# Optimization experiments

Measured on AMD Instinct MI355X. Metric: run time of the kernel, lower is better.

Reference implementation:

```python
import jax, jax.numpy as jnp
import numpy as np

N, V, D, F, E, H = 10000, 4, 3, 128, 320000, 128
EDGE_IN = 2 * F + 2 * V  # node_features[senders] + node_features[receivers] + lengths_x^2 + lengths_y^2
NORM_CONST = 1.0


def setup_inputs() -> dict:
    key = jax.random.key(0)
    ks = jax.random.split(key, 20)
    w = lambda k, shape: jax.random.normal(k, shape, jnp.float32) * 0.05
    z = lambda n: jnp.zeros((n,), jnp.float32)
    return dict(
        node_positions=jax.random.normal(ks[0], (N, V, D), jnp.float32),
        node_vectors=jax.random.normal(ks[1], (N, V, D), jnp.float32),
        node_features=jax.random.normal(ks[2], (N, F), jnp.float32),
        senders=jax.random.randint(ks[3], (E,), 0, N),
        receivers=jax.random.randint(ks[4], (E,), 0, N),
        We0=w(ks[5], (EDGE_IN, H)), be0=z(H), We1=w(ks[6], (H, H)), be1=z(H),
        Winf=w(ks[7], (H, 1)), binf=z(1),
        Wx0=w(ks[8], (H, H)), bx0=z(H), Wx1=w(ks[9], (H, H)), bx1=z(H), Wxf=w(ks[10], (H, V)),
        Wy0=w(ks[11], (H, H)), by0=z(H), Wy1=w(ks[12], (H, H)), by1=z(H), Wyf=w(ks[13], (H, V)),
        Wh0=w(ks[14], (H + F, H)), bh0=z(H), Wh1=w(ks[15], (H, H)), bh1=z(H), Wh2=w(ks[16], (H, F)), bh2=z(F),
    )


def reference(node_positions, node_vectors, node_features, senders, receivers,
              We0, be0, We1, be1, Winf, binf,
              Wx0, bx0, Wx1, bx1, Wxf,
              Wy0, by0, Wy1, by1, Wyf,
              Wh0, bh0, Wh1, bh1, Wh2, bh2):
    act = jax.nn.silu
    n_nodes = node_positions.shape[0]
    avg = int(np.sqrt(receivers.shape[0]))  # avg_num_neighbours as in source

    def radial(coord):  # coord: [N, V, D]
        d = coord[receivers] - coord[senders]              # [E, V, D]
        l = jnp.sqrt(jnp.sum(d * d, axis=-1) + 1e-8)       # [E, V] safe_norm
        d = d / (NORM_CONST + l[:, :, None])               # normalize=True
        return l, d

    lx, dx = radial(node_positions)
    ly, dy = radial(node_vectors)

    ef = jnp.concatenate([node_features[senders], node_features[receivers],
                          lx ** 2, ly ** 2], axis=-1)      # [E, 264]
    m = act(act(ef @ We0 + be0) @ We1 + be1)               # phi_e, activate_final=True

    # phi_x: torso MLP + no-bias head, tanh
    px = jnp.tanh(act(act(m @ Wx0 + bx0) @ Wx1 + bx1) @ Wxf)          # [E, V]
    shifts_x = jax.ops.segment_sum(dx * px[:, :, None], receivers, num_segments=n_nodes) / avg

    # phi_y: torso MLP + no-bias head, tanh
    py = jnp.tanh(act(act(m @ Wy0 + by0) @ Wy1 + by1) @ Wyf)          # [E, V]
    shifts_y = jax.ops.segment_sum(dy * py[:, :, None], receivers, num_segments=n_nodes) / avg

    # attention gate on messages
    m = m * jax.nn.sigmoid(m @ Winf + binf)
    m_i = jax.ops.segment_sum(m, receivers, num_segments=n_nodes) / avg

    # phi_h (activate_final=False) + residual_h
    hin = jnp.concatenate([m_i, node_features], axis=-1)
    features_out = act(act(hin @ Wh0 + bh0) @ Wh1 + bh1) @ Wh2 + bh2 + node_features

    skip = shifts_y
    vectors_out = skip + node_vectors            # residual_y
    positions_out = shifts_x + node_positions    # x_update='x', residual_x
    return positions_out, vectors_out, features_out, skip
```

## Files before the change

### kernel.cpp

```cpp
#include <hip/hip_runtime.h>
#include <math.h>

#define NN 10000
#define EE 320000
#define TE 32
#define INV_AVG (1.0f / 565.0f)

#define OUT_POS 0
#define OUT_VEC 120000
#define OUT_FEAT 240000
#define OUT_SKIP 1520000
#define OUT_TOTAL 1640000

#define WS_WE0 0
#define WS_WE1 36864
#define WS_WX0 53248
#define WS_WX1 69632
#define WS_WY0 86016
#define WS_WY1 102400
#define WS_WH0 118784
#define WS_WH1 151552
#define WS_WH2 167936
#define WS_WXF 184320
#define WS_WYF 186368
#define WS_OFF_NF 376832
#define WS_OFF_SORT 2936832
#define WS_OFF_CNT  4216832
#define WS_OFF_CUR  4256832

typedef __attribute__((ext_vector_type(8))) short bfrag;
typedef __attribute__((ext_vector_type(4))) float f4acc;

__device__ __forceinline__ float siluf(float x) {
    return x * __builtin_amdgcn_rcpf(1.0f + __expf(-x));
}
__device__ __forceinline__ float tanh_fast(float x) {
    return 1.0f - 2.0f * __builtin_amdgcn_rcpf(__expf(2.0f * x) + 1.0f);
}
__device__ __forceinline__ float sigmoid_fast(float x) {
    return __builtin_amdgcn_rcpf(1.0f + __expf(-x));
}
__device__ __forceinline__ unsigned int cvt_pk_bf16(float lo, float hi) {
    unsigned int r;
    asm("v_cvt_pk_bf16_f32 %0, %1, %2" : "=v"(r) : "v"(lo), "v"(hi));
    return r;
}
__device__ __forceinline__ unsigned short f2bf(float x) {
    union { float f; unsigned int u; } c; c.f = x;
    unsigned int r = c.u + 0x7FFFu + ((c.u >> 16) & 1u);
    return (unsigned short)(r >> 16);
}
__device__ __forceinline__ float bf2f(unsigned short h) {
    union { unsigned int u; float f; } c; c.u = ((unsigned int)h) << 16; return c.f;
}

__global__ __launch_bounds__(256) void init_kernel(const float* __restrict__ pos,
                                                   float* __restrict__ out,
                                                   int* __restrict__ cnt)
{
    int idx = blockIdx.x * 256 + threadIdx.x;
    if (idx < OUT_TOTAL) out[idx] = (idx < 120000) ? pos[idx] : 0.0f;
    if (idx < NN) cnt[idx] = 0;
}

__global__ __launch_bounds__(256) void prep_all(
    const float* __restrict__ nf, unsigned short* __restrict__ nfb,
    const int* __restrict__ rcv, int* __restrict__ cnt,
    const float* __restrict__ We0, const float* __restrict__ be0,
    const float* __restrict__ We1,
    const float* __restrict__ Wx0, const float* __restrict__ Wx1,
    const float* __restrict__ Wy0, const float* __restrict__ Wy1,
    const float* __restrict__ Wh0, const float* __restrict__ Wh1,
    const float* __restrict__ Wh2,
    const float* __restrict__ Wxf, const float* __restrict__ Wyf,
    unsigned short* __restrict__ wsW)
{
    int tid = blockIdx.x * 256 + threadIdx.x;
    int i = tid * 8;
    if (i < NN * 128) {
        float4 a = *(const float4*)(nf + i);
        float4 b = *(const float4*)(nf + i + 4);
        uint4 pk;
        pk.x = cvt_pk_bf16(a.x, a.y);
        pk.y = cvt_pk_bf16(a.z, a.w);
        pk.z = cvt_pk_bf16(b.x, b.y);
        pk.w = cvt_pk_bf16(b.z, b.w);
        *(uint4*)(nfb + i) = pk;
    }
    int e = tid * 2;
    if (e < EE) {
        atomicAdd(cnt + rcv[e], 1);
        atomicAdd(cnt + rcv[e + 1], 1);
    }
    if (tid >= 23552) return;
    if (tid >= 23040) {
        const float* Wf = (tid < 23296) ? Wxf : Wyf;
        unsigned short* dst = wsW + ((tid < 23296) ? WS_WXF : WS_WYF);
        int rel = tid - ((tid < 23296) ? 23040 : 23296);
        int kc = rel >> 6, lane = rel & 63;
        int lhi = lane >> 4, llo = lane & 15;
        unsigned short* o = dst + ((kc * 64 + lane) << 3);
#pragma unroll
        for (int j = 0; j < 8; ++j) {
            int k = kc * 32 + lhi * 8 + j;
            o[j] = (llo < 4) ? f2bf(Wf[k * 4 + llo]) : (unsigned short)0;
        }
        return;
    }
    const float* W; unsigned short* dst; int Kact = 128, rel; int isWe0 = 0;
    if (tid < 4608)        { W = We0; dst = wsW + WS_WE0; Kact = 264; rel = tid; isWe0 = 1; }
    else if (tid < 14848)  {
        int r = tid - 4608; int m = r >> 11; rel = r & 2047;
        switch (m) {
            case 0: W = We1; dst = wsW + WS_WE1; break;
            case 1: W = Wx0; dst = wsW + WS_WX0; break;
            case 2: W = Wx1; dst = wsW + WS_WX1; break;
            case 3: W = Wy0; dst = wsW + WS_WY0; break;
            default: W = Wy1; dst = wsW + WS_WY1; break;
        }
    }
    else if (tid < 18944)  { W = Wh0; dst = wsW + WS_WH0; Kact = 256; rel = tid - 14848; }
    else if (tid < 20992)  { W = Wh1; dst = wsW + WS_WH1; rel = tid - 18944; }
    else                   { W = Wh2; dst = wsW + WS_WH2; rel = tid - 20992; }
    int lane = rel & 63, oc = (rel >> 6) & 7, kc = rel >> 9;
    int k0 = kc * 32 + ((lane >> 4) << 3);
    int col = oc * 16 + (lane & 15);
    unsigned short* o = dst + (((kc * 8 + oc) * 64 + lane) << 3);
#pragma unroll
    for (int j = 0; j < 8; ++j) {
        int k = k0 + j;
        unsigned short v = 0;
        if (k < Kact) v = f2bf(W[k * 128 + col]);
        else if (isWe0 && k == 264) v = f2bf(be0[col]);
        o[j] = v;
    }
}

__global__ __launch_bounds__(256) void scan_kernel(const int* __restrict__ cnt,
                                                   int* __restrict__ cursor)
{
    __shared__ int partial[256];
    int t = threadIdx.x;
    int base = t * 40;
    int s = 0;
#pragma unroll 8
    for (int i = 0; i < 40; ++i) { int b = base + i; if (b < NN) s += cnt[b]; }
    partial[t] = s;
    __syncthreads();
    for (int off = 1; off < 256; off <<= 1) {
        int v = 0;
        if (t >= off) v = partial[t - off];
        __syncthreads();
        if (t >= off) partial[t] += v;
        __syncthreads();
    }
    int run = (t ? partial[t - 1] : 0);
    for (int i = 0; i < 40; ++i) {
        int b = base + i;
        if (b < NN) { cursor[b] = run; run += cnt[b]; }
    }
}

__global__ __launch_bounds__(256) void scatter_sort_kernel(const int* __restrict__ rcv,
                                                           int* __restrict__ cursor,
                                                           int* __restrict__ sortedIdx)
{
    int e = blockIdx.x * 256 + threadIdx.x;
    if (e < EE) {
        int slot = atomicAdd(cursor + rcv[e], 1);
        sortedIdx[slot] = e;
    }
}

template<int KC, int MT, int NT>
__device__ __forceinline__ void gemm_lds(const unsigned short* __restrict__ fragW,
                                         const unsigned short* Bld, const int bstride,
                                         const int tile0, const int lane,
                                         f4acc acc[MT][NT])
{
    const int lhi = lane >> 4, llo = lane & 15;
#pragma unroll
    for (int kc = 0; kc < KC; ++kc) {
        bfrag b[NT];
#pragma unroll
        for (int nt = 0; nt < NT; ++nt)
            b[nt] = *(const bfrag*)(Bld + (nt * 16 + llo) * bstride + kc * 32 + lhi * 8);
#pragma unroll
        for (int i = 0; i < MT; ++i) {
            bfrag a = *(const bfrag*)(fragW + (((kc * 8 + tile0 + i) * 64 + lane) << 3));
#pragma unroll
            for (int nt = 0; nt < NT; ++nt)
                acc[i][nt] = __builtin_amdgcn_mfma_f32_16x16x32_bf16(a, b[nt], acc[i][nt], 0, 0, 0);
        }
    }
}

__device__ __forceinline__ void epilogue_silu(f4acc acc[2][2], const float* __restrict__ bias,
                                              unsigned short* Dld, int lane, int w)
{
    const int lhi = lane >> 4, llo = lane & 15;
#pragma unroll
    for (int i = 0; i < 2; ++i) {
        int ch = (w * 2 + i) * 16 + lhi * 4;
        float4 bv = *(const float4*)(bias + ch);
#pragma unroll
        for (int nt = 0; nt < 2; ++nt) {
            uint2 pk;
            pk.x = cvt_pk_bf16(siluf(acc[i][nt][0] + bv.x), siluf(acc[i][nt][1] + bv.y));
            pk.y = cvt_pk_bf16(siluf(acc[i][nt][2] + bv.z), siluf(acc[i][nt][3] + bv.w));
            *(uint2*)(Dld + (nt * 16 + llo) * 136 + ch) = pk;
        }
    }
}

__device__ __forceinline__ void epilogue_silu_nobias(f4acc acc[2][2],
                                                     unsigned short* Dld, int lane, int w)
{
    const int lhi = lane >> 4, llo = lane & 15;
#pragma unroll
    for (int i = 0; i < 2; ++i) {
        int ch = (w * 2 + i) * 16 + lhi * 4;
#pragma unroll
        for (int nt = 0; nt < 2; ++nt) {
            uint2 pk;
            pk.x = cvt_pk_bf16(siluf(acc[i][nt][0]), siluf(acc[i][nt][1]));
            pk.y = cvt_pk_bf16(siluf(acc[i][nt][2]), siluf(acc[i][nt][3]));
            *(uint2*)(Dld + (nt * 16 + llo) * 136 + ch) = pk;
        }
    }
}

__global__ __launch_bounds__(256, 6) void edge_kernel(
    const float* __restrict__ pos, const float* __restrict__ vec,
    const unsigned short* __restrict__ nfb,
    const int* __restrict__ snd, const int* __restrict__ rcv,
    const int* __restrict__ sortedIdx,
    const unsigned short* __restrict__ wsW,
    const float* __restrict__ be1,
    const float* __restrict__ Winf, const float* __restrict__ binf,
    const float* __restrict__ bx0, const float* __restrict__ bx1,
    const float* __restrict__ by0, const float* __restrict__ by1,
    float* outPos, float* outSkip, float* outFeat)
{
    __shared__ unsigned short L2T[TE * 40];
    __shared__ unsigned short H0[TE * 136];
    __shared__ unsigned short Hm[TE * 136];
    __shared__ float dstore[TE * 24];
    __shared__ float pxy[TE * 8];
    __shared__ float gateacc[TE];
    __shared__ int sidx[TE], ridx[TE];

    const int t = threadIdx.x;
    const int lane = t & 63, w = t >> 6;
    const int lhi = lane >> 4, llo = lane & 15;
    const int e_base = blockIdx.x * TE;

    if (t < TE) {
        int eid = sortedIdx[e_base + t];
        int sn = snd[eid], rn = rcv[eid];
        sidx[t] = sn; ridx[t] = rn;
#pragma unroll
        for (int tensor = 0; tensor < 2; ++tensor) {
            const float* c = tensor ? vec : pos;
#pragma unroll
            for (int v = 0; v < 4; ++v) {
                float d0 = c[rn * 12 + v * 3 + 0] - c[sn * 12 + v * 3 + 0];
                float d1 = c[rn * 12 + v * 3 + 1] - c[sn * 12 + v * 3 + 1];
                float d2 = c[rn * 12 + v * 3 + 2] - c[sn * 12 + v * 3 + 2];
                float ss = fmaf(d0, d0, fmaf(d1, d1, d2 * d2)) + 1e-8f;
                float l = sqrtf(ss);
                float inv = __builtin_amdgcn_rcpf(1.0f + l);
                L2T[t * 40 + tensor * 4 + v] = f2bf(ss);
                dstore[t * 24 + tensor * 12 + v * 3 + 0] = d0 * inv;
                dstore[t * 24 + tensor * 12 + v * 3 + 1] = d1 * inv;
                dstore[t * 24 + tensor * 12 + v * 3 + 2] = d2 * inv;
            }
        }
#pragma unroll
        for (int j = 0; j < 6; ++j)
            *(uint2*)(L2T + t * 40 + 8 + j * 4) = make_uint2(0u, 0u);
        L2T[t * 40 + 8] = 0x3F80u;
    }
    if (t >= 64 && t < 96) gateacc[t - 64] = 0.0f;
    __syncthreads();

    {
        const int sn0 = sidx[llo], sn1 = sidx[16 + llo];
        const int rn0 = ridx[llo], rn1 = ridx[16 + llo];
        const unsigned short* s0 = nfb + sn0 * 128 + lhi * 8;
        const unsigned short* s1 = nfb + sn1 * 128 + lhi * 8;
        const unsigned short* r0 = nfb + rn0 * 128 + lhi * 8;
        const unsigned short* r1 = nfb + rn1 * 128 + lhi * 8;
        const int mt0 = w * 2;
        f4acc acc[2][2];
#pragma unroll
        for (int i = 0; i < 2; ++i) { acc[i][0] = (f4acc){0.f,0.f,0.f,0.f}; acc[i][1] = (f4acc){0.f,0.f,0.f,0.f}; }
#pragma unroll
        for (int kc = 0; kc < 8; ++kc) {
            bfrag b0 = *(const bfrag*)((kc < 4 ? s0 : r0) + (kc & 3) * 32);
            bfrag b1 = *(const bfrag*)((kc < 4 ? s1 : r1) + (kc & 3) * 32);
#pragma unroll
            for (int i = 0; i < 2; ++i) {
                bfrag a = *(const bfrag*)(wsW + WS_WE0 + (((kc * 8 + mt0 + i) * 64 + lane) << 3));
                acc[i][0] = __builtin_amdgcn_mfma_f32_16x16x32_bf16(a, b0, acc[i][0], 0, 0, 0);
                acc[i][1] = __builtin_amdgcn_mfma_f32_16x16x32_bf16(a, b1, acc[i][1], 0, 0, 0);
            }
        }
        {
            bfrag b0 = *(const bfrag*)(L2T + llo * 40 + lhi * 8);
            bfrag b1 = *(const bfrag*)(L2T + (16 + llo) * 40 + lhi * 8);
#pragma unroll
            for (int i = 0; i < 2; ++i) {
                bfrag a = *(const bfrag*)(wsW + WS_WE0 + (((8 * 8 + mt0 + i) * 64 + lane) << 3));
                acc[i][0] = __builtin_amdgcn_mfma_f32_16x16x32_bf16(a, b0, acc[i][0], 0, 0, 0);
                acc[i][1] = __builtin_amdgcn_mfma_f32_16x16x32_bf16(a, b1, acc[i][1], 0, 0, 0);
            }
        }
        epilogue_silu_nobias(acc, H0, lane, w);
    }
    __syncthreads();

    {
        f4acc acc[2][2];
#pragma unroll
        for (int i = 0; i < 2; ++i) { acc[i][0] = (f4acc){0.f,0.f,0.f,0.f}; acc[i][1] = (f4acc){0.f,0.f,0.f,0.f}; }
        gemm_lds<4, 2, 2>(wsW + WS_WE1, H0, 136, w * 2, lane, acc);
        float gp0 = 0.0f, gp1 = 0.0f;
#pragma unroll
        for (int i = 0; i < 2; ++i) {
            int ch = (w * 2 + i) * 16 + lhi * 4;
            float4 bv = *(const float4*)(be1 + ch);
            float4 wg = *(const float4*)(Winf + ch);
#pragma unroll
            for (int nt = 0; nt < 2; ++nt) {
                float v0 = siluf(acc[i][nt][0] + bv.x);
                float v1 = siluf(acc[i][nt][1] + bv.y);
                float v2 = siluf(acc[i][nt][2] + bv.z);
                float v3 = siluf(acc[i][nt][3] + bv.w);
                uint2 pk;
                pk.x = cvt_pk_bf16(v0, v1);
                pk.y = cvt_pk_bf16(v2, v3);
                *(uint2*)(Hm + (nt * 16 + llo) * 136 + ch) = pk;
                float g = fmaf(v0, wg.x, fmaf(v1, wg.y, fmaf(v2, wg.z, v3 * wg.w)));
                if (nt == 0) gp0 += g; else gp1 += g;
            }
        }
        gp0 += __shfl_xor(gp0, 16); gp0 += __shfl_xor(gp0, 32);
        gp1 += __shfl_xor(gp1, 16); gp1 += __shfl_xor(gp1, 32);
        if (lane < 16) {
            atomicAdd(&gateacc[lane], gp0);
            atomicAdd(&gateacc[16 + lane], gp1);
        }
    }
    __syncthreads();

#pragma unroll 1
    for (int br = 0; br < 2; ++br) {
        {
            const unsigned short* fw = wsW + (br ? WS_WY0 : WS_WX0);
            const float* bias = br ? by0 : bx0;
            f4acc acc[2][2];
#pragma unroll
            for (int i = 0; i < 2; ++i) { acc[i][0] = (f4acc){0.f,0.f,0.f,0.f}; acc[i][1] = (f4acc){0.f,0.f,0.f,0.f}; }
            gemm_lds<4, 2, 2>(fw, Hm, 136, w * 2, lane, acc);
            epilogue_silu(acc, bias, H0, lane, w);
        }
        __syncthreads();
        {
            const unsigned short* fw = wsW + (br ? WS_WY1 : WS_WX1);
            const float* bias = br ? by1 : bx1;
            f4acc acc[2][2];
#pragma unroll
            for (int i = 0; i < 2; ++i) { acc[i][0] = (f4acc){0.f,0.f,0.f,0.f}; acc[i][1] = (f4acc){0.f,0.f,0.f,0.f}; }
            gemm_lds<4, 2, 2>(fw, H0, 136, w * 2, lane, acc);
            __syncthreads();
            epilogue_silu(acc, bias, H0, lane, w);
        }
        __syncthreads();
        if (w < 2) {
            const unsigned short* fw = wsW + (br ? WS_WYF : WS_WXF);
            f4acc h = (f4acc){0.f, 0.f, 0.f, 0.f};
#pragma unroll
            for (int kc = 0; kc < 4; ++kc) {
                bfrag b = *(const bfrag*)(H0 + (w * 16 + llo) * 136 + kc * 32 + lhi * 8);
                bfrag a = *(const bfrag*)(fw + ((kc * 64 + lane) << 3));
                h = __builtin_amdgcn_mfma_f32_16x16x32_bf16(a, b, h, 0, 0, 0);
            }
            if (lhi == 0) {
#pragma unroll
                for (int v = 0; v < 4; ++v)
                    pxy[(w * 16 + llo) * 8 + br * 4 + v] = h[v];
            }
        }
        __syncthreads();
    }

    pxy[t] = tanh_fast(pxy[t]) * INV_AVG;
    if (t < TE) gateacc[t] = sigmoid_fast(gateacc[t] + binf[0]) * INV_AVG;
    __syncthreads();

    if (t < 128) {
        int half = t >> 6, pair = t & 63;
        int jj = pair * 2;
        int e0h = half * 16;
        float a0 = 0.0f, a1 = 0.0f;
        int prev_r = ridx[e0h];
#pragma unroll
        for (int i = 0; i < 16; ++i) {
            int e = e0h + i;
            int r = ridx[e];
            if (r != prev_r) {
                atomicAdd(outFeat + prev_r * 128 + jj, a0);
                atomicAdd(outFeat + prev_r * 128 + jj + 1, a1);
                a0 = a1 = 0.0f;
                prev_r = r;
            }
            unsigned int pk = *(const unsigned int*)(Hm + e * 136 + jj);
            float g = gateacc[e];
            a0 = fmaf(bf2f((unsigned short)(pk & 0xffffu)), g, a0);
            a1 = fmaf(bf2f((unsigned short)(pk >> 16)), g, a1);
        }
        atomicAdd(outFeat + prev_r * 128 + jj, a0);
        atomicAdd(outFeat + prev_r * 128 + jj + 1, a1);
    } else if (t >= 208) {
        int s = t - 208;
        int c = s >> 1, half = s & 1;
        int tensor = (c >= 12) ? 1 : 0;
        int rem = c - tensor * 12;
        int v = rem / 3;
        float* dstp = tensor ? outSkip : outPos;
        int e0h = half * 16;
        float acc = 0.0f;
        int prev_r = ridx[e0h];
#pragma unroll
        for (int i = 0; i < 16; ++i) {
            int e = e0h + i;
            int r = ridx[e];
            if (r != prev_r) {
                atomicAdd(dstp + prev_r * 12 + rem, acc);
                acc = 0.0f;
                prev_r = r;
            }
            acc = fmaf(dstore[e * 24 + c], pxy[e * 8 + tensor * 4 + v], acc);
        }
        atomicAdd(dstp + prev_r * 12 + rem, acc);
    }
}

__global__ __launch_bounds__(256) void node_kernel(
    const float* __restrict__ nf, const unsigned short* __restrict__ nfb,
    const float* __restrict__ nvec,
    const unsigned short* __restrict__ wsW,
    const float* __restrict__ bh0, const float* __restrict__ bh1,
    const float* __restrict__ bh2,
    float* outFeat , float* outVec,
    const float* __restrict__ outSkip)
{
    __shared__ unsigned short A[TE * 264];
    __shared__ unsigned short H1[TE * 136];
    __shared__ unsigned short H2[TE * 136];
    const int t = threadIdx.x;
    const int lane = t & 63, w = t >> 6;
    const int lhi = lane >> 4, llo = lane & 15;
    const int n_base = blockIdx.x * TE;

#pragma unroll
    for (int it = 0; it < 8; ++it) {
        int idx = t + it * 256;
        int row = idx >> 6, q = idx & 63;
        int n = n_base + row;
        float2 v = make_float2(0.f, 0.f);
        if (n < NN) v = *(const float2*)(outFeat + n * 128 + q * 2);
        *(unsigned int*)(A + row * 264 + q * 2) = cvt_pk_bf16(v.x, v.y);
    }
#pragma unroll
    for (int it = 0; it < 2; ++it) {
        int idx = t + it * 256;
        int row = idx >> 4, q = idx & 15;
        int n = n_base + row;
        uint4 v = make_uint4(0u, 0u, 0u, 0u);
        if (n < NN) v = *(const uint4*)(nfb + n * 128 + q * 8);
        *(uint4*)(A + row * 264 + 128 + q * 8) = v;
    }
    __syncthreads();
    {
        f4acc acc[2][2];
#pragma unroll
        for (int i = 0; i < 2; ++i) { acc[i][0] = (f4acc){0.f,0.f,0.f,0.f}; acc[i][1] = (f4acc){0.f,0.f,0.f,0.f}; }
        gemm_lds<8, 2, 2>(wsW + WS_WH0, A, 264, w * 2, lane, acc);
        epilogue_silu(acc, bh0, H1, lane, w);
    }
    __syncthreads();
    {
        f4acc acc[2][2];
#pragma unroll
        for (int i = 0; i < 2; ++i) { acc[i][0] = (f4acc){0.f,0.f,0.f,0.f}; acc[i][1] = (f4acc){0.f,0.f,0.f,0.f}; }
        gemm_lds<4, 2, 2>(wsW + WS_WH1, H1, 136, w * 2, lane, acc);
        epilogue_silu(acc, bh1, H2, lane, w);
    }
    __syncthreads();
    {
        f4acc acc[2][2];
#pragma unroll
        for (int i = 0; i < 2; ++i) { acc[i][0] = (f4acc){0.f,0.f,0.f,0.f}; acc[i][1] = (f4acc){0.f,0.f,0.f,0.f}; }
        gemm_lds<4, 2, 2>(wsW + WS_WH2, H2, 136, w * 2, lane, acc);
#pragma unroll
        for (int i = 0; i < 2; ++i) {
            int ch = (w * 2 + i) * 16 + lhi * 4;
            float4 bv = *(const float4*)(bh2 + ch);
#pragma unroll
            for (int nt = 0; nt < 2; ++nt) {
                int n = n_base + nt * 16 + llo;
                if (n < NN) {
                    float4 r = *(const float4*)(nf + n * 128 + ch);
                    float4 o;
                    o.x = acc[i][nt][0] + bv.x + r.x;
                    o.y = acc[i][nt][1] + bv.y + r.y;
                    o.z = acc[i][nt][2] + bv.z + r.z;
                    o.w = acc[i][nt][3] + bv.w + r.w;
                    *(float4*)(outFeat + n * 128 + ch) = o;
                }
            }
        }
    }
    {
        int idx = t;
        if (idx < TE * 12) {
            int n = n_base + idx / 12;
            if (n < NN) {
                int g = n_base * 12 + idx;
                outVec[g] = outSkip[g] + nvec[g];
            }
        }
        idx = t + 256;
        if (idx < TE * 12) {
            int n = n_base + idx / 12;
            if (n < NN) {
                int g = n_base * 12 + idx;
                outVec[g] = outSkip[g] + nvec[g];
            }
        }
    }
}

extern "C" void kernel_launch(void* const* d_in, const int* in_sizes, int n_in,
                              void* d_out, int out_size, void* d_ws, size_t ws_size,
                              hipStream_t stream)
{
    (void)in_sizes; (void)n_in; (void)out_size; (void)ws_size;

    const float* pos  = (const float*)d_in[0];
    const float* vecv = (const float*)d_in[1];
    const float* nf   = (const float*)d_in[2];
    const int*   snd  = (const int*)d_in[3];
    const int*   rcv  = (const int*)d_in[4];
    const float* We0  = (const float*)d_in[5];
    const float* be0  = (const float*)d_in[6];
    const float* We1  = (const float*)d_in[7];
    const float* be1  = (const float*)d_in[8];
    const float* Winf = (const float*)d_in[9];
    const float* binf = (const float*)d_in[10];
    const float* Wx0  = (const float*)d_in[11];
    const float* bx0  = (const float*)d_in[12];
    const float* Wx1  = (const float*)d_in[13];
    const float* bx1  = (const float*)d_in[14];
    const float* Wxf  = (const float*)d_in[15];
    const float* Wy0  = (const float*)d_in[16];
    const float* by0  = (const float*)d_in[17];
    const float* Wy1  = (const float*)d_in[18];
    const float* by1  = (const float*)d_in[19];
    const float* Wyf  = (const float*)d_in[20];
    const float* Wh0  = (const float*)d_in[21];
    const float* bh0  = (const float*)d_in[22];
    const float* Wh1  = (const float*)d_in[23];
    const float* bh1  = (const float*)d_in[24];
    const float* Wh2  = (const float*)d_in[25];
    const float* bh2  = (const float*)d_in[26];

    float* out     = (float*)d_out;
    float* outPos  = out + OUT_POS;
    float* outVec  = out + OUT_VEC;
    float* outFeat = out + OUT_FEAT;
    float* outSkip = out + OUT_SKIP;

    char* ws = (char*)d_ws;
    unsigned short* wsW = (unsigned short*)ws;
    unsigned short* nfb = (unsigned short*)(ws + WS_OFF_NF);
    int* sortedIdx      = (int*)(ws + WS_OFF_SORT);
    int* cnt            = (int*)(ws + WS_OFF_CNT);
    int* cursor         = (int*)(ws + WS_OFF_CUR);

    init_kernel<<<(OUT_TOTAL + 255) / 256, 256, 0, stream>>>(pos, out, cnt);

    prep_all<<<(NN * 128 / 8 + 255) / 256, 256, 0, stream>>>(
        nf, nfb, rcv, cnt,
        We0, be0, We1, Wx0, Wx1, Wy0, Wy1, Wh0, Wh1, Wh2, Wxf, Wyf, wsW);

    scan_kernel<<<1, 256, 0, stream>>>(cnt, cursor);
    scatter_sort_kernel<<<(EE + 255) / 256, 256, 0, stream>>>(rcv, cursor, sortedIdx);

    edge_kernel<<<EE / TE, 256, 0, stream>>>(
        pos, vecv, nfb, snd, rcv, sortedIdx, wsW,
        be1, Winf, binf,
        bx0, bx1, by0, by1,
        outPos, outSkip, outFeat);

    node_kernel<<<(NN + TE - 1) / TE, 256, 0, stream>>>(
        nf, nfb, vecv, wsW, bh0, bh1, bh2,
        outFeat, outVec, outSkip);
}
```

Before: 251.2 us.

## Use wave-shuffle scan, unroll edge MLP branches with extra LDS buffer, halve node tile

The single-block scan now runs 1024 threads and uses wave shuffles instead of a barrier-heavy LDS Hillis-Steele loop. In the edge kernel the x/y branch loop is unrolled, and a third LDS buffer removes the mid-GEMM barrier and lets the x head projection overlap with the y first layer. The occupancy hint drops from 6 to 4 blocks per CU. The node kernel tile shrinks from 32 to 16 nodes for more blocks, at the cost of less weight reuse per block.

Measured after the change: 258.7 us. 1.03x slower.

```diff
diff --git a/kernel.cpp b/kernel.cpp
--- a/kernel.cpp
+++ b/kernel.cpp
@@ -4,6 +4,7 @@
 #define NN 10000
 #define EE 320000
 #define TE 32
+#define TN 16
 #define INV_AVG (1.0f / 565.0f)
 
 #define OUT_POS 0
@@ -136,28 +137,45 @@
     }
 }
 
-__global__ __launch_bounds__(256) void scan_kernel(const int* __restrict__ cnt,
-                                                   int* __restrict__ cursor)
-{
-    __shared__ int partial[256];
+__global__ __launch_bounds__(1024) void scan_kernel(const int* __restrict__ cnt,
+                                                    int* __restrict__ cursor)
+{
+    __shared__ int wsum[16];
     int t = threadIdx.x;
-    int base = t * 40;
+    int lane = t & 63, wid = t >> 6;
+    int base = t * 10;
+    int c[10];
     int s = 0;
-#pragma unroll 8
-    for (int i = 0; i < 40; ++i) { int b = base + i; if (b < NN) s += cnt[b]; }
-    partial[t] = s;
-    __syncthreads();
-    for (int off = 1; off < 256; off <<= 1) {
-        int v = 0;
-        if (t >= off) v = partial[t - off];
-        __syncthreads();
-        if (t >= off) partial[t] += v;
-        __syncthreads();
-    }
-    int run = (t ? partial[t - 1] : 0);
-    for (int i = 0; i < 40; ++i) {
+#pragma unroll
+    for (int i = 0; i < 10; ++i) {
         int b = base + i;
-        if (b < NN) { cursor[b] = run; run += cnt[b]; }
+        c[i] = (b < NN) ? cnt[b] : 0;
+        s += c[i];
+    }
+    int run = s;
+#pragma unroll
+    for (int off = 1; off < 64; off <<= 1) {
+        int v = __shfl_up(run, off);
+        if (lane >= off) run += v;
+    }
+    if (lane == 63) wsum[wid] = run;
+    __syncthreads();
+    if (t < 16) {
+        int v = wsum[t];
+#pragma unroll
+        for (int off = 1; off < 16; off <<= 1) {
+            int u = __shfl_up(v, off);
+            if (t >= off) v += u;
+        }
+        wsum[t] = v;
+    }
+    __syncthreads();
+    int wave_excl = (wid == 0) ? 0 : wsum[wid - 1];
+    int excl = wave_excl + run - s;
+#pragma unroll
+    for (int i = 0; i < 10; ++i) {
+        int b = base + i;
+        if (b < NN) { cursor[b] = excl; excl += c[i]; }
     }
 }
 
@@ -195,8 +213,9 @@
     }
 }
 
-__device__ __forceinline__ void epilogue_silu(f4acc acc[2][2], const float* __restrict__ bias,
-                                              unsigned short* Dld, int lane, int w)
+template<int NT>
+__device__ __forceinline__ void epilogue_silu_t(f4acc acc[2][NT], const float* __restrict__ bias,
+                                                unsigned short* Dld, int lane, int w)
 {
     const int lhi = lane >> 4, llo = lane & 15;
 #pragma unroll
@@ -204,7 +223,7 @@
         int ch = (w * 2 + i) * 16 + lhi * 4;
         float4 bv = *(const float4*)(bias + ch);
 #pragma unroll
-        for (int nt = 0; nt < 2; ++nt) {
+        for (int nt = 0; nt < NT; ++nt) {
             uint2 pk;
             pk.x = cvt_pk_bf16(siluf(acc[i][nt][0] + bv.x), siluf(acc[i][nt][1] + bv.y));
             pk.y = cvt_pk_bf16(siluf(acc[i][nt][2] + bv.z), siluf(acc[i][nt][3] + bv.w));
@@ -230,7 +249,7 @@
     }
 }
 
-__global__ __launch_bounds__(256, 6) void edge_kernel(
+__global__ __launch_bounds__(256, 4) void edge_kernel(
     const float* __restrict__ pos, const float* __restrict__ vec,
     const unsigned short* __restrict__ nfb,
     const int* __restrict__ snd, const int* __restrict__ rcv,
@@ -245,6 +264,7 @@
     __shared__ unsigned short L2T[TE * 40];
     __shared__ unsigned short H0[TE * 136];
     __shared__ unsigned short Hm[TE * 136];
+    __shared__ unsigned short H2[TE * 136];
     __shared__ float dstore[TE * 24];
     __shared__ float pxy[TE * 8];
     __shared__ float gateacc[TE];
@@ -354,46 +374,71 @@
     }
     __syncthreads();
 
-#pragma unroll 1
-    for (int br = 0; br < 2; ++br) {
-        {
-            const unsigned short* fw = wsW + (br ? WS_WY0 : WS_WX0);
-            const float* bias = br ? by0 : bx0;
-            f4acc acc[2][2];
-#pragma unroll
-            for (int i = 0; i < 2; ++i) { acc[i][0] = (f4acc){0.f,0.f,0.f,0.f}; acc[i][1] = (f4acc){0.f,0.f,0.f,0.f}; }
-            gemm_lds<4, 2, 2>(fw, Hm, 136, w * 2, lane, acc);
-            epilogue_silu(acc, bias, H0, lane, w);
-        }
-        __syncthreads();
-        {
-            const unsigned short* fw = wsW + (br ? WS_WY1 : WS_WX1);
-            const float* bias = br ? by1 : bx1;
-            f4acc acc[2][2];
-#pragma unroll
-            for (int i = 0; i < 2; ++i) { acc[i][0] = (f4acc){0.f,0.f,0.f,0.f}; acc[i][1] = (f4acc){0.f,0.f,0.f,0.f}; }
-            gemm_lds<4, 2, 2>(fw, H0, 136, w * 2, lane, acc);
-            __syncthreads();
-            epilogue_silu(acc, bias, H0, lane, w);
-        }
-        __syncthreads();
+    {
+        f4acc acc[2][2];
+#pragma unroll
+        for (int i = 0; i < 2; ++i) { acc[i][0] = (f4acc){0.f,0.f,0.f,0.f}; acc[i][1] = (f4acc){0.f,0.f,0.f,0.f}; }
+        gemm_lds<4, 2, 2>(wsW + WS_WX0, Hm, 136, w * 2, lane, acc);
+        epilogue_silu_t<2>(acc, bx0, H0, lane, w);
+    }
+    __syncthreads();
+
+    {
+        f4acc acc[2][2];
+#pragma unroll
+        for (int i = 0; i < 2; ++i) { acc[i][0] = (f4acc){0.f,0.f,0.f,0.f}; acc[i][1] = (f4acc){0.f,0.f,0.f,0.f}; }
+        gemm_lds<4, 2, 2>(wsW + WS_WX1, H0, 136, w * 2, lane, acc);
+        epilogue_silu_t<2>(acc, bx1, H2, lane, w);
+    }
+    __syncthreads();
+
+    {
+        f4acc acc[2][2];
+#pragma unroll
+        for (int i = 0; i < 2; ++i) { acc[i][0] = (f4acc){0.f,0.f,0.f,0.f}; acc[i][1] = (f4acc){0.f,0.f,0.f,0.f}; }
+        gemm_lds<4, 2, 2>(wsW + WS_WY0, Hm, 136, w * 2, lane, acc);
+        epilogue_silu_t<2>(acc, by0, H0, lane, w);
         if (w < 2) {
-            const unsigned short* fw = wsW + (br ? WS_WYF : WS_WXF);
             f4acc h = (f4acc){0.f, 0.f, 0.f, 0.f};
 #pragma unroll
             for (int kc = 0; kc < 4; ++kc) {
-                bfrag b = *(const bfrag*)(H0 + (w * 16 + llo) * 136 + kc * 32 + lhi * 8);
-                bfrag a = *(const bfrag*)(fw + ((kc * 64 + lane) << 3));
+                bfrag b = *(const bfrag*)(H2 + (w * 16 + llo) * 136 + kc * 32 + lhi * 8);
+                bfrag a = *(const bfrag*)(wsW + WS_WXF + ((kc * 64 + lane) << 3));
                 h = __builtin_amdgcn_mfma_f32_16x16x32_bf16(a, b, h, 0, 0, 0);
             }
             if (lhi == 0) {
 #pragma unroll
                 for (int v = 0; v < 4; ++v)
-                    pxy[(w * 16 + llo) * 8 + br * 4 + v] = h[v];
-            }
-        }
-        __syncthreads();
-    }
+                    pxy[(w * 16 + llo) * 8 + v] = h[v];
+            }
+        }
+    }
+    __syncthreads();
+
+    {
+        f4acc acc[2][2];
+#pragma unroll
+        for (int i = 0; i < 2; ++i) { acc[i][0] = (f4acc){0.f,0.f,0.f,0.f}; acc[i][1] = (f4acc){0.f,0.f,0.f,0.f}; }
+        gemm_lds<4, 2, 2>(wsW + WS_WY1, H0, 136, w * 2, lane, acc);
+        epilogue_silu_t<2>(acc, by1, H2, lane, w);
+    }
+    __syncthreads();
+
+    if (w < 2) {
+        f4acc h = (f4acc){0.f, 0.f, 0.f, 0.f};
+#pragma unroll
+        for (int kc = 0; kc < 4; ++kc) {
+            bfrag b = *(const bfrag*)(H2 + (w * 16 + llo) * 136 + kc * 32 + lhi * 8);
+            bfrag a = *(const bfrag*)(wsW + WS_WYF + ((kc * 64 + lane) << 3));
+            h = __builtin_amdgcn_mfma_f32_16x16x32_bf16(a, b, h, 0, 0, 0);
+        }
+        if (lhi == 0) {
+#pragma unroll
+            for (int v = 0; v < 4; ++v)
+                pxy[(w * 16 + llo) * 8 + 4 + v] = h[v];
+        }
+    }
+    __syncthreads();
 
     pxy[t] = tanh_fast(pxy[t]) * INV_AVG;
     if (t < TE) gateacc[t] = sigmoid_fast(gateacc[t] + binf[0]) * INV_AVG;
@@ -456,16 +501,16 @@
     float* outFeat , float* outVec,
     const float* __restrict__ outSkip)
 {
-    __shared__ unsigned short A[TE * 264];
-    __shared__ unsigned short H1[TE * 136];
-    __shared__ unsigned short H2[TE * 136];
+    __shared__ unsigned short A[TN * 264];
+    __shared__ unsigned short H1[TN * 136];
+    __shared__ unsigned short H2b[TN * 136];
     const int t = threadIdx.x;
     const int lane = t & 63, w = t >> 6;
     const int lhi = lane >> 4, llo = lane & 15;
-    const int n_base = blockIdx.x * TE;
-
-#pragma unroll
-    for (int it = 0; it < 8; ++it) {
+    const int n_base = blockIdx.x * TN;
+
+#pragma unroll
+    for (int it = 0; it < 4; ++it) {
         int idx = t + it * 256;
         int row = idx >> 6, q = idx & 63;
         int n = n_base + row;
@@ -473,10 +518,8 @@
         if (n < NN) v = *(const float2*)(outFeat + n * 128 + q * 2);
         *(unsigned int*)(A + row * 264 + q * 2) = cvt_pk_bf16(v.x, v.y);
     }
-#pragma unroll
-    for (int it = 0; it < 2; ++it) {
-        int idx = t + it * 256;
-        int row = idx >> 4, q = idx & 15;
+    {
+        int row = t >> 4, q = t & 15;
         int n = n_base + row;
         uint4 v = make_uint4(0u, 0u, 0u, 0u);
         if (n < NN) v = *(const uint4*)(nfb + n * 128 + q * 8);
@@ -484,61 +527,44 @@
     }
     __syncthreads();
     {
-        f4acc acc[2][2];
-#pragma unroll
-        for (int i = 0; i < 2; ++i) { acc[i][0] = (f4acc){0.f,0.f,0.f,0.f}; acc[i][1] = (f4acc){0.f,0.f,0.f,0.f}; }
-        gemm_lds<8, 2, 2>(wsW + WS_WH0, A, 264, w * 2, lane, acc);
-        epilogue_silu(acc, bh0, H1, lane, w);
-    }
-    __syncthreads();
-    {
-        f4acc acc[2][2];
-#pragma unroll
-        for (int i = 0; i < 2; ++i) { acc[i][0] = (f4acc){0.f,0.f,0.f,0.f}; acc[i][1] = (f4acc){0.f,0.f,0.f,0.f}; }
-        gemm_lds<4, 2, 2>(wsW + WS_WH1, H1, 136, w * 2, lane, acc);
-        epilogue_silu(acc, bh1, H2, lane, w);
-    }
-    __syncthreads();
-    {
-        f4acc acc[2][2];
-#pragma unroll
-        for (int i = 0; i < 2; ++i) { acc[i][0] = (f4acc){0.f,0.f,0.f,0.f}; acc[i][1] = (f4acc){0.f,0.f,0.f,0.f}; }
-        gemm_lds<4, 2, 2>(wsW + WS_WH2, H2, 136, w * 2, lane, acc);
+        f4acc acc[2][1];
+        acc[0][0] = (f4acc){0.f,0.f,0.f,0.f}; acc[1][0] = (f4acc){0.f,0.f,0.f,0.f};
+        gemm_lds<8, 2, 1>(wsW + WS_WH0, A, 264, w * 2, lane, acc);
+        epilogue_silu_t<1>(acc, bh0, H1, lane, w);
+    }
+    __syncthreads();
+    {
+        f4acc acc[2][1];
+        acc[0][0] = (f4acc){0.f,0.f,0.f,0.f}; acc[1][0] = (f4acc){0.f,0.f,0.f,0.f};
+        gemm_lds<4, 2, 1>(wsW + WS_WH1, H1, 136, w * 2, lane, acc);
+        epilogue_silu_t<1>(acc, bh1, H2b, lane, w);
+    }
+    __syncthreads();
+    {
+        f4acc acc[2][1];
+        acc[0][0] = (f4acc){0.f,0.f,0.f,0.f}; acc[1][0] = (f4acc){0.f,0.f,0.f,0.f};
+        gemm_lds<4, 2, 1>(wsW + WS_WH2, H2b, 136, w * 2, lane, acc);
 #pragma unroll
         for (int i = 0; i < 2; ++i) {
             int ch = (w * 2 + i) * 16 + lhi * 4;
             float4 bv = *(const float4*)(bh2 + ch);
-#pragma unroll
-            for (int nt = 0; nt < 2; ++nt) {
-                int n = n_base + nt * 16 + llo;
-                if (n < NN) {
-                    float4 r = *(const float4*)(nf + n * 128 + ch);
-                    float4 o;
-                    o.x = acc[i][nt][0] + bv.x + r.x;
-                    o.y = acc[i][nt][1] + bv.y + r.y;
-                    o.z = acc[i][nt][2] + bv.z + r.z;
-                    o.w = acc[i][nt][3] + bv.w + r.w;
-                    *(float4*)(outFeat + n * 128 + ch) = o;
-                }
-            }
-        }
-    }
-    {
-        int idx = t;
-        if (idx < TE * 12) {
-            int n = n_base + idx / 12;
+            int n = n_base + llo;
             if (n < NN) {
-                int g = n_base * 12 + idx;
-                outVec[g] = outSkip[g] + nvec[g];
-            }
-        }
-        idx = t + 256;
-        if (idx < TE * 12) {
-            int n = n_base + idx / 12;
-            if (n < NN) {
-                int g = n_base * 12 + idx;
-                outVec[g] = outSkip[g] + nvec[g];
-            }
+                float4 r = *(const float4*)(nf + n * 128 + ch);
+                float4 o;
+                o.x = acc[i][0][0] + bv.x + r.x;
+                o.y = acc[i][0][1] + bv.y + r.y;
+                o.z = acc[i][0][2] + bv.z + r.z;
+                o.w = acc[i][0][3] + bv.w + r.w;
+                *(float4*)(outFeat + n * 128 + ch) = o;
+            }
+        }
+    }
+    if (t < TN * 12) {
+        int n = n_base + t / 12;
+        if (n < NN) {
+            int g = n_base * 12 + t;
+            outVec[g] = outSkip[g] + nvec[g];
         }
     }
 }
@@ -596,7 +622,7 @@
         nf, nfb, rcv, cnt,
         We0, be0, We1, Wx0, Wx1, Wy0, Wy1, Wh0, Wh1, Wh2, Wxf, Wyf, wsW);
 
-    scan_kernel<<<1, 256, 0, stream>>>(cnt, cursor);
+    scan_kernel<<<1, 1024, 0, stream>>>(cnt, cursor);
     scatter_sort_kernel<<<(EE + 255) / 256, 256, 0, stream>>>(rcv, cursor, sortedIdx);
 
     edge_kernel<<<EE / TE, 256, 0, stream>>>(
@@ -605,7 +631,7 @@
         bx0, bx1, by0, by1,
         outPos, outSkip, outFeat);
 
-    node_kernel<<<(NN + TE - 1) / TE, 256, 0, stream>>>(
+    node_kernel<<<(NN + TN - 1) / TN, 256, 0, stream>>>(
         nf, nfb, vecv, wsW, bh0, bh1, bh2,
         outFeat, outVec, outSkip);
 }
```
